# Optimization experiments

Measured on AMD Instinct MI355X. Metric: run time of the kernel, lower is better.

The kernel has to match this reference:

```python
import jax, jax.numpy as jnp
import numpy as np

L = 12        # num_layers == seq_len
HORIZON = 6


def setup_inputs() -> dict:
    key = jax.random.key(0)
    k0, k1, k2, k3, k4 = jax.random.split(key, 5)
    B, N, T = 64, 1024, 12
    x = jax.random.normal(k0, (B, 1, N, T), jnp.float32)
    # hidden_size=1 -> PyTorch init is U(-1,1); use scaled normals
    w_ih = jax.random.normal(k1, (L, 3), jnp.float32) * 0.5
    w_hh = jax.random.normal(k2, (L, 3), jnp.float32) * 0.5
    b_ih = jax.random.normal(k3, (L, 3), jnp.float32) * 0.5
    b_hh = jax.random.normal(k4, (L, 3), jnp.float32) * 0.5
    return {"x": x, "w_ih": w_ih, "w_hh": w_hh, "b_ih": b_ih, "b_hh": b_hh}


def _gru_pass(seq, h0, w_ih, w_hh, b_ih, b_hh):
    # seq: [T, B, N] scalar inputs per step; h0: [L, B, N]
    def step(h, x_t):
        inp = x_t                       # [B, N]
        new_h = []
        for l in range(L):
            gi = inp[..., None] * w_ih[l] + b_ih[l]      # [B, N, 3]
            gh = h[l][..., None] * w_hh[l] + b_hh[l]     # [B, N, 3]
            r = jax.nn.sigmoid(gi[..., 0] + gh[..., 0])
            z = jax.nn.sigmoid(gi[..., 1] + gh[..., 1])
            n = jnp.tanh(gi[..., 2] + r * gh[..., 2])
            hn = (1.0 - z) * n + z * h[l]
            new_h.append(hn)
            inp = hn                    # output of layer l feeds layer l+1
        return jnp.stack(new_h), inp    # carry [L,B,N], top-layer output [B,N]
    h_final, outs = jax.lax.scan(step, h0, seq)
    return outs, h_final                # outs: [T, B, N]


def reference(x, w_ih, w_hh, b_ih, b_hh):
    # x: [B, 1, N, T]  (permute(0,2,3,1) in torch -> [B, N, T, 1])
    B, _, N, T = x.shape
    seq = jnp.transpose(x[:, 0], (2, 0, 1))   # [T, B, N]
    h = jnp.zeros((L, B, N), x.dtype)          # hidden=None -> zeros
    outs, h = _gru_pass(seq, h, w_ih, w_hh, b_ih, b_hh)
    for _ in range(HORIZON):
        outs, h = _gru_pass(outs, h, w_ih, w_hh, b_ih, b_hh)
    # torch builds result[i] = final hidden of layer i, shaped [B,1,N,1];
    # we return the stacked list: [L, B, 1, N, 1]
    return h[:, :, None, :, None]
```

## Files before the change

kernel.cpp:

```cpp
#include <hip/hip_runtime.h>

#define LNUM 12
#define TNUM 12
#define NPASS 7

__global__ void gru_prep_kernel(const float* __restrict__ w_ih,
                                const float* __restrict__ w_hh,
                                const float* __restrict__ b_ih,
                                const float* __restrict__ b_hh,
                                float* __restrict__ ws) {
    const float NL2E = -1.4426950408889634f;
    const float TL2E =  2.8853900817779268f;
    int j = threadIdx.x;
    if (j >= 10 * LNUM) return;
    int g = j / LNUM, l = j % LNUM;
    float v;
    switch (g) {
        case 0: v = NL2E * w_ih[3*l+0]; break;
        case 1: v = NL2E * w_ih[3*l+1]; break;
        case 2: v = TL2E * w_ih[3*l+2]; break;
        case 3: v = NL2E * w_hh[3*l+0]; break;
        case 4: v = NL2E * w_hh[3*l+1]; break;
        case 5: v = TL2E * w_hh[3*l+2]; break;
        case 6: v = NL2E * (b_ih[3*l+0] + b_hh[3*l+0]); break;
        case 7: v = NL2E * (b_ih[3*l+1] + b_hh[3*l+1]); break;
        case 8: v = TL2E * b_ih[3*l+2]; break;
        default: v = TL2E * b_hh[3*l+2]; break;
    }
    ws[j] = v;
}

__global__ __launch_bounds__(256, 1)
void gru_chain_kernel(const float* __restrict__ x,
                      const float* __restrict__ ws,
                      float* __restrict__ out,
                      int total) {
    const int tid = blockIdx.x * blockDim.x + threadIdx.x;
    if (tid >= total) return;

    const float* __restrict__ wi0 = ws +   0;
    const float* __restrict__ wi1 = ws +  12;
    const float* __restrict__ wi2 = ws +  24;
    const float* __restrict__ wh0 = ws +  36;
    const float* __restrict__ wh1 = ws +  48;
    const float* __restrict__ wh2 = ws +  60;

    float vb0[LNUM], vb1[LNUM], vbi2[LNUM], vbh2[LNUM];
#pragma unroll
    for (int l = 0; l < LNUM; ++l) {
        vb0[l]  = ws[72  + l];
        vb1[l]  = ws[84  + l];
        vbi2[l] = ws[96  + l];
        vbh2[l] = ws[108 + l];
    }

    float seq[TNUM];
    const float4* xv = reinterpret_cast<const float4*>(x + (size_t)tid * TNUM);
#pragma unroll
    for (int i = 0; i < TNUM / 4; ++i) {
        float4 v = xv[i];
        seq[i*4+0] = v.x; seq[i*4+1] = v.y; seq[i*4+2] = v.z; seq[i*4+3] = v.w;
    }

    float h[LNUM];
#pragma unroll
    for (int l = 0; l < LNUM; ++l) h[l] = 0.0f;

#pragma unroll 1
    for (int p = 0; p < NPASS; ++p) {
#pragma unroll
        for (int t = 0; t < TNUM; ++t) {
            float inp = seq[t];
#pragma unroll
            for (int l = 0; l < LNUM; ++l) {
                float ar = fmaf(inp, wi0[l], fmaf(h[l], wh0[l], vb0[l]));
                float az = fmaf(inp, wi1[l], fmaf(h[l], wh1[l], vb1[l]));
                float gn = fmaf(inp, wi2[l], vbi2[l]);
                float hg = fmaf(h[l], wh2[l], vbh2[l]);

                float er = __builtin_amdgcn_exp2f(ar);
                float ez = __builtin_amdgcn_exp2f(az);
                float ea = 1.0f + er;
                float eb = 1.0f + ez;
                float D  = __builtin_amdgcn_rcpf(ea * eb);
                float r  = D * eb;
                float z  = D * ea;

                float en = __builtin_amdgcn_exp2f(fmaf(r, hg, gn));
                float u  = __builtin_amdgcn_rcpf(1.0f + en);
                float n  = fmaf(-2.0f, u, 1.0f);

                float hn = fmaf(z, h[l], fmaf(-z, n, n));
                h[l] = hn;
                inp  = hn;
            }
            seq[t] = inp;
        }
    }

#pragma unroll
    for (int l = 0; l < LNUM; ++l) {
        out[(size_t)l * total + tid] = h[l];
    }
}

extern "C" void kernel_launch(void* const* d_in, const int* in_sizes, int n_in,
                              void* d_out, int out_size, void* d_ws, size_t ws_size,
                              hipStream_t stream) {
    const float* x    = (const float*)d_in[0];
    const float* w_ih = (const float*)d_in[1];
    const float* w_hh = (const float*)d_in[2];
    const float* b_ih = (const float*)d_in[3];
    const float* b_hh = (const float*)d_in[4];
    float* out = (float*)d_out;
    float* ws  = (float*)d_ws;

    gru_prep_kernel<<<1, 128, 0, stream>>>(w_ih, w_hh, b_ih, b_hh, ws);

    const int total = in_sizes[0] / TNUM;
    const int block = 256;
    const int grid  = (total + block - 1) / block;
    gru_chain_kernel<<<grid, block, 0, stream>>>(x, ws, out, total);
}
```

Baseline: 111.0 us.

## Pipeline GRU layers across two wavefronts via shared-memory handoff

Splits the 12-layer chain into two 6-layer halves run by two wavefronts per block, which pass activations through a shared-memory double buffer and a ring buffer across time steps and passes. This doubles the number of wavefronts working on the serial dependency chain (systolic layer pipelining), giving more parallelism and latency hiding for the same total chains. It adds a __syncthreads per time step and shared-memory traffic, and it assumes total is a multiple of 64 with no bounds check.

```diff
diff --git a/kernel.cpp b/kernel.cpp
--- a/kernel.cpp
+++ b/kernel.cpp
@@ -3,6 +3,8 @@
 #define LNUM 12
 #define TNUM 12
 #define NPASS 7
+#define GL 6
+#define CPB 64
 
 __global__ void gru_prep_kernel(const float* __restrict__ w_ih,
                                 const float* __restrict__ w_hh,
@@ -30,77 +32,114 @@
     ws[j] = v;
 }
 
-__global__ __launch_bounds__(256, 1)
-void gru_chain_kernel(const float* __restrict__ x,
-                      const float* __restrict__ ws,
-                      float* __restrict__ out,
-                      int total) {
-    const int tid = blockIdx.x * blockDim.x + threadIdx.x;
-    if (tid >= total) return;
+template<int BASE>
+__device__ __forceinline__ void load_bias(const float* __restrict__ ws,
+                                          float (&bias)[4 * GL]) {
+#pragma unroll
+    for (int i = 0; i < GL; ++i) {
+        float b0  = ws[72  + BASE + i];
+        float b1  = ws[84  + BASE + i];
+        float bi2 = ws[96  + BASE + i];
+        float bh2 = ws[108 + BASE + i];
+        asm volatile("" : "+v"(b0), "+v"(b1), "+v"(bi2), "+v"(bh2));
+        bias[4*i+0] = b0; bias[4*i+1] = b1; bias[4*i+2] = bi2; bias[4*i+3] = bh2;
+    }
+}
 
-    const float* __restrict__ wi0 = ws +   0;
-    const float* __restrict__ wi1 = ws +  12;
-    const float* __restrict__ wi2 = ws +  24;
-    const float* __restrict__ wh0 = ws +  36;
-    const float* __restrict__ wh1 = ws +  48;
-    const float* __restrict__ wh2 = ws +  60;
+template<int BASE>
+__device__ __forceinline__ float step6(const float* __restrict__ ws,
+                                       const float (&bias)[4 * GL],
+                                       float (&h)[GL], float inp) {
+#pragma unroll
+    for (int i = 0; i < GL; ++i) {
+        const float wi0 = ws[ 0 + BASE + i];
+        const float wi1 = ws[12 + BASE + i];
+        const float wi2 = ws[24 + BASE + i];
+        const float wh0 = ws[36 + BASE + i];
+        const float wh1 = ws[48 + BASE + i];
+        const float wh2 = ws[60 + BASE + i];
 
-    float vb0[LNUM], vb1[LNUM], vbi2[LNUM], vbh2[LNUM];
+        float ar = fmaf(inp, wi0, fmaf(h[i], wh0, bias[4*i+0]));
+        float az = fmaf(inp, wi1, fmaf(h[i], wh1, bias[4*i+1]));
+        float gn = fmaf(inp, wi2, bias[4*i+2]);
+        float hg = fmaf(h[i], wh2, bias[4*i+3]);
+
+        float er = __builtin_amdgcn_exp2f(ar);
+        float ez = __builtin_amdgcn_exp2f(az);
+        float ea = 1.0f + er;
+        float eb = 1.0f + ez;
+        float D  = __builtin_amdgcn_rcpf(ea * eb);
+        float r  = D * eb;
+        float z  = D * ea;
+
+        float en = __builtin_amdgcn_exp2f(fmaf(r, hg, gn));
+        float u  = __builtin_amdgcn_rcpf(1.0f + en);
+        float n  = fmaf(-2.0f, u, 1.0f);
+
+        float hn = fmaf(z, h[i], fmaf(-z, n, n));
+        h[i] = hn;
+        inp  = hn;
+    }
+    return inp;
+}
+
+__global__ __launch_bounds__(128, 2)
+void gru_sys_kernel(const float* __restrict__ x,
+                    const float* __restrict__ ws,
+                    float* __restrict__ out,
+                    int total) {
+    __shared__ float ring[TNUM][CPB];
+    __shared__ float hand[2][CPB];
+
+    const int  lane  = threadIdx.x & 63;
+    const bool g0    = threadIdx.x < 64;
+    const int  chain = blockIdx.x * CPB + lane;
+
+    float h[GL];
 #pragma unroll
-    for (int l = 0; l < LNUM; ++l) {
-        vb0[l]  = ws[72  + l];
-        vb1[l]  = ws[84  + l];
-        vbi2[l] = ws[96  + l];
-        vbh2[l] = ws[108 + l];
+    for (int i = 0; i < GL; ++i) h[i] = 0.0f;
+
+    float bias[4 * GL];
+    float seq[TNUM];
+    if (g0) {
+        load_bias<0>(ws, bias);
+        const float4* xv = reinterpret_cast<const float4*>(x + (size_t)chain * TNUM);
+#pragma unroll
+        for (int i = 0; i < TNUM / 4; ++i) {
+            float4 v = xv[i];
+            seq[i*4+0] = v.x; seq[i*4+1] = v.y; seq[i*4+2] = v.z; seq[i*4+3] = v.w;
+        }
+    } else {
+        load_bias<GL>(ws, bias);
     }
-
-    float seq[TNUM];
-    const float4* xv = reinterpret_cast<const float4*>(x + (size_t)tid * TNUM);
-#pragma unroll
-    for (int i = 0; i < TNUM / 4; ++i) {
-        float4 v = xv[i];
-        seq[i*4+0] = v.x; seq[i*4+1] = v.y; seq[i*4+2] = v.z; seq[i*4+3] = v.w;
-    }
-
-    float h[LNUM];
-#pragma unroll
-    for (int l = 0; l < LNUM; ++l) h[l] = 0.0f;
 
 #pragma unroll 1
     for (int p = 0; p < NPASS; ++p) {
 #pragma unroll
         for (int t = 0; t < TNUM; ++t) {
-            float inp = seq[t];
-#pragma unroll
-            for (int l = 0; l < LNUM; ++l) {
-                float ar = fmaf(inp, wi0[l], fmaf(h[l], wh0[l], vb0[l]));
-                float az = fmaf(inp, wi1[l], fmaf(h[l], wh1[l], vb1[l]));
-                float gn = fmaf(inp, wi2[l], vbi2[l]);
-                float hg = fmaf(h[l], wh2[l], vbh2[l]);
-
-                float er = __builtin_amdgcn_exp2f(ar);
-                float ez = __builtin_amdgcn_exp2f(az);
-                float ea = 1.0f + er;
-                float eb = 1.0f + ez;
-                float D  = __builtin_amdgcn_rcpf(ea * eb);
-                float r  = D * eb;
-                float z  = D * ea;
-
-                float en = __builtin_amdgcn_exp2f(fmaf(r, hg, gn));
-                float u  = __builtin_amdgcn_rcpf(1.0f + en);
-                float n  = fmaf(-2.0f, u, 1.0f);
-
-                float hn = fmaf(z, h[l], fmaf(-z, n, n));
-                h[l] = hn;
-                inp  = hn;
+            if (g0) {
+                float inp = (p == 0) ? seq[t] : ring[t][lane];
+                float h5  = step6<0>(ws, bias, h, inp);
+                hand[t & 1][lane] = h5;
+            } else {
+                if (t > 0 || p > 0) {
+                    float inp = hand[(t + 1) & 1][lane];
+                    float top = step6<GL>(ws, bias, h, inp);
+                    ring[(t + 11) % 12][lane] = top;
+                }
             }
-            seq[t] = inp;
+            __syncthreads();
         }
     }
+    if (!g0) {
+        float inp = hand[1][lane];
+        (void)step6<GL>(ws, bias, h, inp);
+    }
 
+    const int base_l = g0 ? 0 : GL;
 #pragma unroll
-    for (int l = 0; l < LNUM; ++l) {
-        out[(size_t)l * total + tid] = h[l];
+    for (int i = 0; i < GL; ++i) {
+        out[(size_t)(base_l + i) * total + chain] = h[i];
     }
 }
 
@@ -118,7 +157,6 @@
     gru_prep_kernel<<<1, 128, 0, stream>>>(w_ih, w_hh, b_ih, b_hh, ws);
 
     const int total = in_sizes[0] / TNUM;
-    const int block = 256;
-    const int grid  = (total + block - 1) / block;
-    gru_chain_kernel<<<grid, block, 0, stream>>>(x, ws, out, total);
+    const int grid  = total / CPB;
+    gru_sys_kernel<<<grid, 128, 0, stream>>>(x, ws, out, total);
 }
```

After: 118.4 us. 6.7% more time.

## Reorder GRU recurrence into layer/time wavefront diagonals for instruction-level parallelism

Applied to the files above, without the earlier changes.

The per-thread recurrence is restructured from a sequential time-then-layer loop into a wavefront over diagonals. Each diagonal updates all 12 layers at once, since each layer only depends on the previous diagonal's values, so the dependency chains become independent. The chain across passes works because the top output at step t feeds layer 0 twelve diagonals later. The kernel also holds all weights in registers with asm barriers that stop them being rematerialised, which raises register pressure in exchange for hiding exp/rcp latency.

```diff
diff --git a/kernel.cpp b/kernel.cpp
--- a/kernel.cpp
+++ b/kernel.cpp
@@ -30,28 +30,47 @@
     ws[j] = v;
 }
 
+__device__ __forceinline__ float cell(const float (&W)[10][LNUM],
+                                      float (&h)[LNUM], const int l, float inp) {
+    float ar = fmaf(inp,  W[0][l], fmaf(h[l], W[3][l], W[6][l]));
+    float az = fmaf(inp,  W[1][l], fmaf(h[l], W[4][l], W[7][l]));
+    float gn = fmaf(inp,  W[2][l], W[8][l]);
+    float hg = fmaf(h[l], W[5][l], W[9][l]);
+
+    float er = __builtin_amdgcn_exp2f(ar);
+    float ez = __builtin_amdgcn_exp2f(az);
+    float ea = 1.0f + er;
+    float eb = 1.0f + ez;
+    float D  = __builtin_amdgcn_rcpf(ea * eb);
+    float r  = D * eb;
+    float z  = D * ea;
+
+    float en = __builtin_amdgcn_exp2f(fmaf(r, hg, gn));
+    float u  = __builtin_amdgcn_rcpf(1.0f + en);
+    float n  = fmaf(-2.0f, u, 1.0f);
+
+    float hn = fmaf(z, h[l], fmaf(-z, n, n));
+    h[l] = hn;
+    return hn;
+}
+
 __global__ __launch_bounds__(256, 1)
-void gru_chain_kernel(const float* __restrict__ x,
-                      const float* __restrict__ ws,
-                      float* __restrict__ out,
-                      int total) {
+void gru_diag_kernel(const float* __restrict__ x,
+                     const float* __restrict__ ws,
+                     float* __restrict__ out,
+                     int total) {
     const int tid = blockIdx.x * blockDim.x + threadIdx.x;
     if (tid >= total) return;
 
-    const float* __restrict__ wi0 = ws +   0;
-    const float* __restrict__ wi1 = ws +  12;
-    const float* __restrict__ wi2 = ws +  24;
-    const float* __restrict__ wh0 = ws +  36;
-    const float* __restrict__ wh1 = ws +  48;
-    const float* __restrict__ wh2 = ws +  60;
-
-    float vb0[LNUM], vb1[LNUM], vbi2[LNUM], vbh2[LNUM];
+    float W[10][LNUM];
 #pragma unroll
-    for (int l = 0; l < LNUM; ++l) {
-        vb0[l]  = ws[72  + l];
-        vb1[l]  = ws[84  + l];
-        vbi2[l] = ws[96  + l];
-        vbh2[l] = ws[108 + l];
+    for (int g = 0; g < 10; ++g) {
+#pragma unroll
+        for (int l = 0; l < LNUM; ++l) {
+            float w = ws[g * LNUM + l];
+            asm volatile("" : "+v"(w));
+            W[g][l] = w;
+        }
     }
 
     float seq[TNUM];
@@ -66,35 +85,30 @@
 #pragma unroll
     for (int l = 0; l < LNUM; ++l) h[l] = 0.0f;
 
+#pragma unroll
+    for (int d = 0; d < 12; ++d) {
+#pragma unroll
+        for (int l = 11; l >= 1; --l) {
+            if (l <= d) h[l] = cell(W, h, l, h[l - 1]);
+        }
+        h[0] = cell(W, h, 0, seq[d]);
+    }
+
 #pragma unroll 1
-    for (int p = 0; p < NPASS; ++p) {
+    for (int d = 12; d < 84; ++d) {
+        float top = h[11];
 #pragma unroll
-        for (int t = 0; t < TNUM; ++t) {
-            float inp = seq[t];
+        for (int l = 11; l >= 1; --l) {
+            h[l] = cell(W, h, l, h[l - 1]);
+        }
+        h[0] = cell(W, h, 0, top);
+    }
+
 #pragma unroll
-            for (int l = 0; l < LNUM; ++l) {
-                float ar = fmaf(inp, wi0[l], fmaf(h[l], wh0[l], vb0[l]));
-                float az = fmaf(inp, wi1[l], fmaf(h[l], wh1[l], vb1[l]));
-                float gn = fmaf(inp, wi2[l], vbi2[l]);
-                float hg = fmaf(h[l], wh2[l], vbh2[l]);
-
-                float er = __builtin_amdgcn_exp2f(ar);
-                float ez = __builtin_amdgcn_exp2f(az);
-                float ea = 1.0f + er;
-                float eb = 1.0f + ez;
-                float D  = __builtin_amdgcn_rcpf(ea * eb);
-                float r  = D * eb;
-                float z  = D * ea;
-
-                float en = __builtin_amdgcn_exp2f(fmaf(r, hg, gn));
-                float u  = __builtin_amdgcn_rcpf(1.0f + en);
-                float n  = fmaf(-2.0f, u, 1.0f);
-
-                float hn = fmaf(z, h[l], fmaf(-z, n, n));
-                h[l] = hn;
-                inp  = hn;
-            }
-            seq[t] = inp;
+    for (int d = 84; d < 95; ++d) {
+#pragma unroll
+        for (int l = 11; l >= 1; --l) {
+            if (l >= d - 83) h[l] = cell(W, h, l, h[l - 1]);
         }
     }
 
@@ -120,5 +134,5 @@
     const int total = in_sizes[0] / TNUM;
     const int block = 256;
     const int grid  = (total + block - 1) / block;
-    gru_chain_kernel<<<grid, block, 0, stream>>>(x, ws, out, total);
+    gru_diag_kernel<<<grid, block, 0, stream>>>(x, ws, out, total);
 }
```

Result: no change. 110.5 us (-0.4%).
